# Kernel optimization log

Measured on AMD Instinct MI355X. Metric: run time of the kernel, lower is better.

Reference implementation:

```python
import jax, jax.numpy as jnp
import numpy as np

NUM_GRAPHS = 1024

def setup_inputs() -> dict:
    key = jax.random.key(0)
    k1, k2, k3, k4 = jax.random.split(key, 4)
    N, D, H = 200000, 512, 128
    h = jax.random.normal(k1, (N, D), dtype=jnp.float32)
    batch = jnp.sort(jax.random.randint(k2, (N,), 0, NUM_GRAPHS)).astype(jnp.int32)
    # gate MLP params: Linear(D,H) -> tanh -> Linear(H,1)
    W1 = jax.random.normal(k3, (D, H), dtype=jnp.float32) / np.sqrt(D)
    b1 = jnp.zeros((H,), dtype=jnp.float32)
    W2 = jax.random.normal(k4, (H, 1), dtype=jnp.float32) / np.sqrt(H)
    b2 = jnp.zeros((1,), dtype=jnp.float32)
    return {"h": h, "batch": batch, "W1": W1, "b1": b1, "W2": W2, "b2": b2}

def reference(h, batch, W1, b1, W2, b2):
    # gate MLP -> per-node logit
    logits = (jnp.tanh(h @ W1 + b1) @ W2 + b2)[:, 0]  # [N]
    # segment softmax over nodes within each graph
    seg_max = jax.ops.segment_max(logits, batch, num_segments=NUM_GRAPHS,
                                  indices_are_sorted=True)  # [G]
    ex = jnp.exp(logits - seg_max[batch])  # [N]
    denom = jax.ops.segment_sum(ex, batch, num_segments=NUM_GRAPHS,
                                indices_are_sorted=True)  # [G]
    a = ex / denom[batch]  # [N]
    # weighted scatter-add pooling
    pooled = jax.ops.segment_sum(h * a[:, None], batch, num_segments=NUM_GRAPHS,
                                 indices_are_sorted=True)  # [G, D]
    return pooled
```

## Files before the change

### kernel.cpp

```cpp
#include <hip/hip_runtime.h>
#include <hip/hip_bf16.h>

typedef __attribute__((ext_vector_type(8))) short short8;
typedef __attribute__((ext_vector_type(4))) float f32x4;

#define NGRAPHS 1024
#define D_DIM 512
#define H_DIM 128
#define BM 32
#define BMA 64

static __device__ __forceinline__ unsigned int pack_bf2(float a, float b) {
    float2 t; t.x = a; t.y = b;
    __hip_bfloat162 h = __float22bfloat162_rn(t);
    union { __hip_bfloat162 h; unsigned int u; } v;
    v.h = h;
    return v.u;
}

static __device__ __forceinline__ unsigned short f2bf(float f) {
    __hip_bfloat16 h = __float2bfloat16(f);
    union { __hip_bfloat16 h; unsigned short u; } v;
    v.h = h;
    return v.u;
}

static __device__ __forceinline__ float fast_tanh(float x) {
    float cx = fminf(fmaxf(x, -15.f), 15.f);
    float e = __expf(2.f * cx);
    return (e - 1.f) / (e + 1.f);
}

__global__ void seg_offsets_kernel(const int* __restrict__ batch, int N,
                                   int* __restrict__ off) {
    int g = blockIdx.x * 256 + threadIdx.x;
    if (g > NGRAPHS) return;
    int lo = 0, hi = N;
    while (lo < hi) {
        int mid = (lo + hi) >> 1;
        if (batch[mid] < g) lo = mid + 1;
        else hi = mid;
    }
    off[g] = lo;
}

__global__ void prep_w1t_kernel(const float* __restrict__ W1,
                                unsigned short* __restrict__ W1TF) {
    int idx = blockIdx.x * 256 + threadIdx.x;
    int e = idx & 7;
    int lane = (idx >> 3) & 63;
    int ki = (idx >> 9) & 15;
    int cgrp = idx >> 13;
    int col = cgrp * 16 + (lane & 15);
    int k = ki * 32 + (lane >> 4) * 8 + e;
    W1TF[idx] = f2bf(W1[k * H_DIM + col]);
}

__global__ __launch_bounds__(256, 4) void gate_pool_partial_kernel(
    const float* __restrict__ h, const unsigned short* __restrict__ W1TF,
    const float* __restrict__ b1, const float* __restrict__ W2,
    const int* __restrict__ batch, float* __restrict__ P,
    float* __restrict__ out, int N) {
    __shared__ unsigned short hA[BM * D_DIM];
    __shared__ float plds[4][BM];
    __shared__ float wl[BM];
    __shared__ int gb[BM];

    const int tid = threadIdx.x;
    const int lane = tid & 63;
    const int w = tid >> 6;
    const int cg = lane & 15;
    const int qg = lane >> 4;
    const int row0 = blockIdx.x * BM;

    if (tid < BM) {
        int gr = row0 + tid;
        gb[tid] = batch[gr < N ? gr : N - 1];
    }

#pragma unroll
    for (int bb = 0; bb < 2; ++bb) {
        float4 f[8];
#pragma unroll
        for (int i = 0; i < 8; ++i) {
            const int task = (bb * 8 + i) * 4 + w;
            const int row = task >> 1, half = task & 1;
            int gr = row0 + row;
            gr = gr < N ? gr : N - 1;
            f[i] = *(const float4*)(h + (size_t)gr * D_DIM + half * 256 + lane * 4);
        }
        __builtin_amdgcn_sched_barrier(0);
#pragma unroll
        for (int i = 0; i < 8; ++i) {
            const int task = (bb * 8 + i) * 4 + w;
            const int row = task >> 1, half = task & 1;
            const int unit = half * 32 + (lane >> 1);
            uint2 v;
            v.x = pack_bf2(f[i].x, f[i].y);
            v.y = pack_bf2(f[i].z, f[i].w);
            *(uint2*)&hA[row * D_DIM + ((unit ^ (row & 7)) * 8) + (lane & 1) * 4] = v;
        }
    }
    __syncthreads();

    f32x4 acc[2][2];
#pragma unroll
    for (int rf = 0; rf < 2; ++rf)
#pragma unroll
        for (int cf = 0; cf < 2; ++cf) acc[rf][cf] = (f32x4){0.f, 0.f, 0.f, 0.f};
#pragma unroll
    for (int ki = 0; ki < 16; ++ki) {
        short8 bfg[2];
#pragma unroll
        for (int cf = 0; cf < 2; ++cf)
            bfg[cf] = *(const short8*)(W1TF +
                (((w * 2 + cf) * 16 + ki) << 9) + lane * 8);
#pragma unroll
        for (int rf = 0; rf < 2; ++rf) {
            const short8 af = *(const short8*)&hA[(rf * 16 + cg) * D_DIM +
                (((4 * ki + qg) ^ (cg & 7)) * 8)];
#pragma unroll
            for (int cf = 0; cf < 2; ++cf)
                acc[rf][cf] = __builtin_amdgcn_mfma_f32_16x16x32_bf16(
                    bfg[cf], af, acc[rf][cf], 0, 0, 0);
        }
    }

    float4 b1v[2], w2v[2];
#pragma unroll
    for (int cf = 0; cf < 2; ++cf) {
        b1v[cf] = *(const float4*)&b1[(w * 2 + cf) * 16 + qg * 4];
        w2v[cf] = *(const float4*)&W2[(w * 2 + cf) * 16 + qg * 4];
    }
#pragma unroll
    for (int rf = 0; rf < 2; ++rf) {
        float p = 0.f;
#pragma unroll
        for (int cf = 0; cf < 2; ++cf) {
            p += fast_tanh(acc[rf][cf][0] + b1v[cf].x) * w2v[cf].x;
            p += fast_tanh(acc[rf][cf][1] + b1v[cf].y) * w2v[cf].y;
            p += fast_tanh(acc[rf][cf][2] + b1v[cf].z) * w2v[cf].z;
            p += fast_tanh(acc[rf][cf][3] + b1v[cf].w) * w2v[cf].w;
        }
        p += __shfl_xor(p, 16, 64);
        p += __shfl_xor(p, 32, 64);
        if (qg == 0) plds[w][rf * 16 + cg] = p;
    }
    __syncthreads();

    if (tid < BM) {
        const float l = plds[0][tid] + plds[1][tid] + plds[2][tid] + plds[3][tid];
        wl[tid] = (row0 + tid < N) ? __expf(fminf(l, 60.f)) : 0.f;
    }
    __syncthreads();

    {
        const int d0 = (tid >> 2) * 8 + (tid & 3) * 2;
        float ax = 0.f, ay = 0.f, d = 0.f;
        int curg = gb[0];
#pragma unroll 8
        for (int j = 0; j < BM; ++j) {
            const int gj = gb[j];
            if (gj != curg) {
                if (curg == gb[0]) {
                    float* rec = P + (size_t)blockIdx.x * 2 * 513;
                    rec[d0] = ax; rec[d0 + 1] = ay;
                    if (tid == 0) rec[512] = d;
                } else {
                    out[(size_t)curg * D_DIM + d0] = ax / d;
                    out[(size_t)curg * D_DIM + d0 + 1] = ay / d;
                }
                ax = 0.f; ay = 0.f; d = 0.f; curg = gj;
            }
            const float wj = wl[j];
            const unsigned int pair = *(const unsigned int*)&hA[j * D_DIM +
                (((tid >> 2) ^ (j & 7)) * 8) + (tid & 3) * 2];
            ax += wj * __uint_as_float(pair << 16);
            ay += wj * __uint_as_float(pair & 0xffff0000u);
            d += wj;
        }
        const int slot = (curg == gb[0]) ? 0 : 1;
        float* rec = P + ((size_t)blockIdx.x * 2 + slot) * 513;
        rec[d0] = ax; rec[d0 + 1] = ay;
        if (tid == 0) rec[512] = d;
        if (gb[0] == gb[BM - 1]) {
            float* r1 = P + ((size_t)blockIdx.x * 2 + 1) * 513;
            r1[d0] = 0.f; r1[d0 + 1] = 0.f;
            if (tid == 0) r1[512] = 0.f;
        }
    }
}

__global__ __launch_bounds__(512) void reduce_kernel(
    const float* __restrict__ P, const int* __restrict__ off,
    const int* __restrict__ batch, float* __restrict__ out, int N) {
    const int g = blockIdx.x;
    const int tid = threadIdx.x;
    const int s = off[g], e = off[g + 1];
    if (e <= s) { out[(size_t)g * D_DIM + tid] = 0.f; return; }
    const int t0 = s >> 5, t1 = (e - 1) >> 5;
    float sum = 0.f, den = 0.f;
    bool found = false;
    for (int b = t0; b <= t1; ++b) {
        const int fg = batch[b << 5];
        const int le = (b << 5) + 31;
        const int lg = batch[le < N ? le : N - 1];
        if (fg == g) {
            const float* rec = P + (size_t)b * 2 * 513;
            sum += rec[tid]; den += rec[512]; found = true;
        } else if (lg == g) {
            const float* rec = P + ((size_t)b * 2 + 1) * 513;
            sum += rec[tid]; den += rec[512]; found = true;
        }
    }
    if (found) out[(size_t)g * D_DIM + tid] = sum / den;
}

__global__ void zero_kernel(float* __restrict__ out, float* __restrict__ den) {
    int i = blockIdx.x * 256 + threadIdx.x;
    if (i < NGRAPHS * D_DIM) out[i] = 0.f;
    if (i < NGRAPHS) den[i] = 0.f;
}

__global__ __launch_bounds__(256) void gate_pool_atomic_kernel(
    const float* __restrict__ h, const unsigned short* __restrict__ W1TF,
    const float* __restrict__ b1, const float* __restrict__ W2,
    const int* __restrict__ batch, float* __restrict__ outnum,
    float* __restrict__ den, int N) {
    __shared__ unsigned short hA[BMA * D_DIM];
    __shared__ float plds[4][BMA];
    __shared__ float wl[BMA];
    __shared__ int gb[BMA];

    const int tid = threadIdx.x;
    const int lane = tid & 63;
    const int w = tid >> 6;
    const int cg = lane & 15;
    const int qg = lane >> 4;
    const int row0 = blockIdx.x * BMA;

    if (tid < BMA) {
        int gr = row0 + tid;
        gb[tid] = batch[gr < N ? gr : N - 1];
    }
#pragma unroll
    for (int b = 0; b < 4; ++b) {
        float4 fa[4], fb[4];
#pragma unroll
        for (int i = 0; i < 4; ++i) {
            const int fi = (b * 4 + i) * 256 + tid;
            const int r = fi >> 6, u = fi & 63;
            int gr = row0 + r;
            gr = gr < N ? gr : N - 1;
            const float* p = h + (size_t)gr * D_DIM + u * 8;
            fa[i] = *(const float4*)p;
            fb[i] = *(const float4*)(p + 4);
        }
#pragma unroll
        for (int i = 0; i < 4; ++i) {
            const int fi = (b * 4 + i) * 256 + tid;
            const int r = fi >> 6, u = fi & 63;
            uint4 val;
            val.x = pack_bf2(fa[i].x, fa[i].y);
            val.y = pack_bf2(fa[i].z, fa[i].w);
            val.z = pack_bf2(fb[i].x, fb[i].y);
            val.w = pack_bf2(fb[i].z, fb[i].w);
            *(uint4*)&hA[r * D_DIM + ((u ^ (r & 7)) * 8)] = val;
        }
    }
    __syncthreads();

    f32x4 acc[4][2];
#pragma unroll
    for (int rf = 0; rf < 4; ++rf)
#pragma unroll
        for (int cf = 0; cf < 2; ++cf) acc[rf][cf] = (f32x4){0.f, 0.f, 0.f, 0.f};
#pragma unroll
    for (int ki = 0; ki < 16; ++ki) {
        short8 bfg[2];
#pragma unroll
        for (int cf = 0; cf < 2; ++cf)
            bfg[cf] = *(const short8*)(W1TF + (((w * 2 + cf) * 16 + ki) << 9) + lane * 8);
#pragma unroll
        for (int rf = 0; rf < 4; ++rf) {
            const int row = rf * 16 + cg;
            const short8 af = *(const short8*)&hA[row * D_DIM +
                (((4 * ki + qg) ^ (row & 7)) * 8)];
#pragma unroll
            for (int cf = 0; cf < 2; ++cf)
                acc[rf][cf] = __builtin_amdgcn_mfma_f32_16x16x32_bf16(
                    af, bfg[cf], acc[rf][cf], 0, 0, 0);
        }
    }
    const float b1v0 = b1[w * 32 + cg];
    const float b1v1 = b1[w * 32 + 16 + cg];
    const float w2v0 = W2[w * 32 + cg];
    const float w2v1 = W2[w * 32 + 16 + cg];
#pragma unroll
    for (int rf = 0; rf < 4; ++rf) {
#pragma unroll
        for (int reg = 0; reg < 4; ++reg) {
            float p = fast_tanh(acc[rf][0][reg] + b1v0) * w2v0 +
                      fast_tanh(acc[rf][1][reg] + b1v1) * w2v1;
#pragma unroll
            for (int o = 1; o < 16; o <<= 1) p += __shfl_xor(p, o, 64);
            if (cg == 0) plds[w][rf * 16 + qg * 4 + reg] = p;
        }
    }
    __syncthreads();
    if (tid < BMA) {
        const float l = plds[0][tid] + plds[1][tid] + plds[2][tid] + plds[3][tid];
        wl[tid] = (row0 + tid < N) ? __expf(fminf(l, 60.f)) : 0.f;
    }
    __syncthreads();

    const int d0 = (tid >> 2) * 8 + (tid & 3) * 2;
    float ax = 0.f, ay = 0.f;
    int cur = gb[0];
#pragma unroll 8
    for (int j = 0; j < BMA; ++j) {
        const int gj = gb[j];
        if (gj != cur) {
            atomicAdd(&outnum[(size_t)cur * D_DIM + d0], ax);
            atomicAdd(&outnum[(size_t)cur * D_DIM + d0 + 1], ay);
            ax = 0.f; ay = 0.f; cur = gj;
        }
        const float wj = wl[j];
        const unsigned int pair = *(const unsigned int*)&hA[j * D_DIM +
            (((tid >> 2) ^ (j & 7)) * 8) + (tid & 3) * 2];
        ax += wj * __uint_as_float(pair << 16);
        ay += wj * __uint_as_float(pair & 0xffff0000u);
    }
    atomicAdd(&outnum[(size_t)cur * D_DIM + d0], ax);
    atomicAdd(&outnum[(size_t)cur * D_DIM + d0 + 1], ay);

    if (tid == 0) {
        float a = 0.f;
        int c2 = gb[0];
        for (int j = 0; j < BMA; ++j) {
            if (gb[j] != c2) { atomicAdd(&den[c2], a); a = 0.f; c2 = gb[j]; }
            a += wl[j];
        }
        atomicAdd(&den[c2], a);
    }
}

__global__ __launch_bounds__(512) void finalize_kernel(
    float* __restrict__ out, const float* __restrict__ den) {
    const int g = blockIdx.x;
    const float dv = den[g];
    const float v = out[(size_t)g * D_DIM + threadIdx.x];
    out[(size_t)g * D_DIM + threadIdx.x] = dv > 0.f ? v / dv : 0.f;
}

extern "C" void kernel_launch(void* const* d_in, const int* in_sizes, int n_in,
                              void* d_out, int out_size, void* d_ws, size_t ws_size,
                              hipStream_t stream) {
    const float* h = (const float*)d_in[0];
    const int* batch = (const int*)d_in[1];
    const float* W1 = (const float*)d_in[2];
    const float* b1 = (const float*)d_in[3];
    const float* W2 = (const float*)d_in[4];
    float* out = (float*)d_out;
    const int N = in_sizes[1];
    const int NB = (N + BM - 1) / BM;

    char* ws = (char*)d_ws;
    int* off = (int*)ws;
    unsigned short* W1TF = (unsigned short*)(ws + 4608);
    float* P = (float*)(ws + 135680);

    const size_t need = 135680 + (size_t)NB * 2 * 513 * 4;

    seg_offsets_kernel<<<(NGRAPHS + 256) / 256 + 1, 256, 0, stream>>>(batch, N, off);
    prep_w1t_kernel<<<(D_DIM * H_DIM) / 256, 256, 0, stream>>>(W1, W1TF);

    if (ws_size >= need) {
        gate_pool_partial_kernel<<<NB, 256, 0, stream>>>(h, W1TF, b1, W2, batch,
                                                         P, out, N);
        reduce_kernel<<<NGRAPHS, 512, 0, stream>>>(P, off, batch, out, N);
    } else {
        float* den = P;
        zero_kernel<<<(NGRAPHS * D_DIM + 255) / 256, 256, 0, stream>>>(out, den);
        gate_pool_atomic_kernel<<<(N + BMA - 1) / BMA, 256, 0, stream>>>(
            h, W1TF, b1, W2, batch, out, den, N);
        finalize_kernel<<<NGRAPHS, 512, 0, stream>>>(out, den);
    }
}
```

Measured before the change: 138.4 us.

## Process two row tiles per block, prefetching second tile during first's compute

Each block now handles two consecutive 32-row tiles. It issues global loads for the second tile's h rows into registers while the first tile's MFMA gate and pooling run, then commits them to LDS. The goal is to hide HBM latency behind compute in a memory-bound kernel. In exchange, 64 extra float registers are held per thread across the MFMA phase, which may lower occupancy under the launch bounds, and the grid is halved.

```diff
diff --git a/kernel.cpp b/kernel.cpp
--- a/kernel.cpp
+++ b/kernel.cpp
@@ -56,11 +56,125 @@
     W1TF[idx] = f2bf(W1[k * H_DIM + col]);
 }
 
-__global__ __launch_bounds__(256, 4) void gate_pool_partial_kernel(
+static __device__ __forceinline__ void stage_issue8(
+    const float* __restrict__ h, int N, int row0, int bb, int w, int lane,
+    float4* f) {
+#pragma unroll
+    for (int i = 0; i < 8; ++i) {
+        const int task = (bb * 8 + i) * 4 + w;
+        const int row = task >> 1, half = task & 1;
+        int gr = row0 + row;
+        gr = gr < N ? gr : N - 1;
+        f[i] = *(const float4*)(h + (size_t)gr * D_DIM + half * 256 + lane * 4);
+    }
+}
+
+static __device__ __forceinline__ void stage_commit8(
+    unsigned short* __restrict__ hA, int bb, int w, int lane, const float4* f) {
+#pragma unroll
+    for (int i = 0; i < 8; ++i) {
+        const int task = (bb * 8 + i) * 4 + w;
+        const int row = task >> 1, half = task & 1;
+        const int unit = half * 32 + (lane >> 1);
+        uint2 v;
+        v.x = pack_bf2(f[i].x, f[i].y);
+        v.y = pack_bf2(f[i].z, f[i].w);
+        *(uint2*)&hA[row * D_DIM + ((unit ^ (row & 7)) * 8) + (lane & 1) * 4] = v;
+    }
+}
+
+static __device__ __forceinline__ void do_mfma_epi(
+    const unsigned short* __restrict__ hA, const unsigned short* __restrict__ W1TF,
+    const float* __restrict__ b1, const float* __restrict__ W2,
+    float (*plds)[BM], int w, int lane, int cg, int qg) {
+    f32x4 acc[2][2];
+#pragma unroll
+    for (int rf = 0; rf < 2; ++rf)
+#pragma unroll
+        for (int cf = 0; cf < 2; ++cf) acc[rf][cf] = (f32x4){0.f, 0.f, 0.f, 0.f};
+#pragma unroll
+    for (int ki = 0; ki < 16; ++ki) {
+        short8 bfg[2];
+#pragma unroll
+        for (int cf = 0; cf < 2; ++cf)
+            bfg[cf] = *(const short8*)(W1TF +
+                (((w * 2 + cf) * 16 + ki) << 9) + lane * 8);
+#pragma unroll
+        for (int rf = 0; rf < 2; ++rf) {
+            const short8 af = *(const short8*)&hA[(rf * 16 + cg) * D_DIM +
+                (((4 * ki + qg) ^ (cg & 7)) * 8)];
+#pragma unroll
+            for (int cf = 0; cf < 2; ++cf)
+                acc[rf][cf] = __builtin_amdgcn_mfma_f32_16x16x32_bf16(
+                    bfg[cf], af, acc[rf][cf], 0, 0, 0);
+        }
+    }
+    float4 b1v[2], w2v[2];
+#pragma unroll
+    for (int cf = 0; cf < 2; ++cf) {
+        b1v[cf] = *(const float4*)&b1[(w * 2 + cf) * 16 + qg * 4];
+        w2v[cf] = *(const float4*)&W2[(w * 2 + cf) * 16 + qg * 4];
+    }
+#pragma unroll
+    for (int rf = 0; rf < 2; ++rf) {
+        float p = 0.f;
+#pragma unroll
+        for (int cf = 0; cf < 2; ++cf) {
+            p += fast_tanh(acc[rf][cf][0] + b1v[cf].x) * w2v[cf].x;
+            p += fast_tanh(acc[rf][cf][1] + b1v[cf].y) * w2v[cf].y;
+            p += fast_tanh(acc[rf][cf][2] + b1v[cf].z) * w2v[cf].z;
+            p += fast_tanh(acc[rf][cf][3] + b1v[cf].w) * w2v[cf].w;
+        }
+        p += __shfl_xor(p, 16, 64);
+        p += __shfl_xor(p, 32, 64);
+        if (qg == 0) plds[w][rf * 16 + cg] = p;
+    }
+}
+
+static __device__ __forceinline__ void do_pool_flush(
+    const unsigned short* __restrict__ hA, const float* __restrict__ wl,
+    const int* __restrict__ gb, float* __restrict__ P, float* __restrict__ out,
+    int t, int tid) {
+    const int d0 = (tid >> 2) * 8 + (tid & 3) * 2;
+    float ax = 0.f, ay = 0.f, d = 0.f;
+    int curg = gb[0];
+#pragma unroll 8
+    for (int j = 0; j < BM; ++j) {
+        const int gj = gb[j];
+        if (gj != curg) {
+            if (curg == gb[0]) {
+                float* rec = P + (size_t)t * 2 * 513;
+                rec[d0] = ax; rec[d0 + 1] = ay;
+                if (tid == 0) rec[512] = d;
+            } else {
+                out[(size_t)curg * D_DIM + d0] = ax / d;
+                out[(size_t)curg * D_DIM + d0 + 1] = ay / d;
+            }
+            ax = 0.f; ay = 0.f; d = 0.f; curg = gj;
+        }
+        const float wj = wl[j];
+        const unsigned int pair = *(const unsigned int*)&hA[j * D_DIM +
+            (((tid >> 2) ^ (j & 7)) * 8) + (tid & 3) * 2];
+        ax += wj * __uint_as_float(pair << 16);
+        ay += wj * __uint_as_float(pair & 0xffff0000u);
+        d += wj;
+    }
+    const int slot = (curg == gb[0]) ? 0 : 1;
+    float* rec = P + ((size_t)t * 2 + slot) * 513;
+    rec[d0] = ax; rec[d0 + 1] = ay;
+    if (tid == 0) rec[512] = d;
+    if (gb[0] == gb[BM - 1]) {
+        float* r1 = P + ((size_t)t * 2 + 1) * 513;
+        r1[d0] = 0.f; r1[d0 + 1] = 0.f;
+        if (tid == 0) r1[512] = 0.f;
+    }
+}
+
+__global__ __launch_bounds__(256, 4) void gate_pool_pipe_kernel(
     const float* __restrict__ h, const unsigned short* __restrict__ W1TF,
     const float* __restrict__ b1, const float* __restrict__ W2,
     const int* __restrict__ batch, float* __restrict__ P,
-    float* __restrict__ out, int N) {
+    float* __restrict__ out, int N, int NBtot) {
     __shared__ unsigned short hA[BM * D_DIM];
     __shared__ float plds[4][BM];
     __shared__ float wl[BM];
@@ -71,124 +185,71 @@
     const int w = tid >> 6;
     const int cg = lane & 15;
     const int qg = lane >> 4;
-    const int row0 = blockIdx.x * BM;
+
+    const int tA = blockIdx.x * 2;
+    if (tA >= NBtot) return;
+    const int tB = tA + 1;
+    const bool haveB = tB < NBtot;
+    const int row0A = tA * BM;
+    const int row0B = tB * BM;
 
     if (tid < BM) {
-        int gr = row0 + tid;
+        int gr = row0A + tid;
         gb[tid] = batch[gr < N ? gr : N - 1];
     }
 
-#pragma unroll
-    for (int bb = 0; bb < 2; ++bb) {
+    {
         float4 f[8];
-#pragma unroll
-        for (int i = 0; i < 8; ++i) {
-            const int task = (bb * 8 + i) * 4 + w;
-            const int row = task >> 1, half = task & 1;
-            int gr = row0 + row;
-            gr = gr < N ? gr : N - 1;
-            f[i] = *(const float4*)(h + (size_t)gr * D_DIM + half * 256 + lane * 4);
-        }
+        stage_issue8(h, N, row0A, 0, w, lane, f);
         __builtin_amdgcn_sched_barrier(0);
-#pragma unroll
-        for (int i = 0; i < 8; ++i) {
-            const int task = (bb * 8 + i) * 4 + w;
-            const int row = task >> 1, half = task & 1;
-            const int unit = half * 32 + (lane >> 1);
-            uint2 v;
-            v.x = pack_bf2(f[i].x, f[i].y);
-            v.y = pack_bf2(f[i].z, f[i].w);
-            *(uint2*)&hA[row * D_DIM + ((unit ^ (row & 7)) * 8) + (lane & 1) * 4] = v;
-        }
-    }
-    __syncthreads();
-
-    f32x4 acc[2][2];
-#pragma unroll
-    for (int rf = 0; rf < 2; ++rf)
-#pragma unroll
-        for (int cf = 0; cf < 2; ++cf) acc[rf][cf] = (f32x4){0.f, 0.f, 0.f, 0.f};
-#pragma unroll
-    for (int ki = 0; ki < 16; ++ki) {
-        short8 bfg[2];
-#pragma unroll
-        for (int cf = 0; cf < 2; ++cf)
-            bfg[cf] = *(const short8*)(W1TF +
-                (((w * 2 + cf) * 16 + ki) << 9) + lane * 8);
-#pragma unroll
-        for (int rf = 0; rf < 2; ++rf) {
-            const short8 af = *(const short8*)&hA[(rf * 16 + cg) * D_DIM +
-                (((4 * ki + qg) ^ (cg & 7)) * 8)];
-#pragma unroll
-            for (int cf = 0; cf < 2; ++cf)
-                acc[rf][cf] = __builtin_amdgcn_mfma_f32_16x16x32_bf16(
-                    bfg[cf], af, acc[rf][cf], 0, 0, 0);
-        }
-    }
-
-    float4 b1v[2], w2v[2];
-#pragma unroll
-    for (int cf = 0; cf < 2; ++cf) {
-        b1v[cf] = *(const float4*)&b1[(w * 2 + cf) * 16 + qg * 4];
-        w2v[cf] = *(const float4*)&W2[(w * 2 + cf) * 16 + qg * 4];
-    }
-#pragma unroll
-    for (int rf = 0; rf < 2; ++rf) {
-        float p = 0.f;
-#pragma unroll
-        for (int cf = 0; cf < 2; ++cf) {
-            p += fast_tanh(acc[rf][cf][0] + b1v[cf].x) * w2v[cf].x;
-            p += fast_tanh(acc[rf][cf][1] + b1v[cf].y) * w2v[cf].y;
-            p += fast_tanh(acc[rf][cf][2] + b1v[cf].z) * w2v[cf].z;
-            p += fast_tanh(acc[rf][cf][3] + b1v[cf].w) * w2v[cf].w;
-        }
-        p += __shfl_xor(p, 16, 64);
-        p += __shfl_xor(p, 32, 64);
-        if (qg == 0) plds[w][rf * 16 + cg] = p;
-    }
+        stage_commit8(hA, 0, w, lane, f);
+    }
+    {
+        float4 f[8];
+        stage_issue8(h, N, row0A, 1, w, lane, f);
+        __builtin_amdgcn_sched_barrier(0);
+        stage_commit8(hA, 1, w, lane, f);
+    }
+    __syncthreads();
+
+    float4 pf0[8], pf1[8];
+    if (haveB) stage_issue8(h, N, row0B, 0, w, lane, pf0);
+    __builtin_amdgcn_sched_barrier(0);
+
+    do_mfma_epi(hA, W1TF, b1, W2, plds, w, lane, cg, qg);
     __syncthreads();
 
     if (tid < BM) {
         const float l = plds[0][tid] + plds[1][tid] + plds[2][tid] + plds[3][tid];
-        wl[tid] = (row0 + tid < N) ? __expf(fminf(l, 60.f)) : 0.f;
-    }
-    __syncthreads();
-
-    {
-        const int d0 = (tid >> 2) * 8 + (tid & 3) * 2;
-        float ax = 0.f, ay = 0.f, d = 0.f;
-        int curg = gb[0];
-#pragma unroll 8
-        for (int j = 0; j < BM; ++j) {
-            const int gj = gb[j];
-            if (gj != curg) {
-                if (curg == gb[0]) {
-                    float* rec = P + (size_t)blockIdx.x * 2 * 513;
-                    rec[d0] = ax; rec[d0 + 1] = ay;
-                    if (tid == 0) rec[512] = d;
-                } else {
-                    out[(size_t)curg * D_DIM + d0] = ax / d;
-                    out[(size_t)curg * D_DIM + d0 + 1] = ay / d;
-                }
-                ax = 0.f; ay = 0.f; d = 0.f; curg = gj;
-            }
-            const float wj = wl[j];
-            const unsigned int pair = *(const unsigned int*)&hA[j * D_DIM +
-                (((tid >> 2) ^ (j & 7)) * 8) + (tid & 3) * 2];
-            ax += wj * __uint_as_float(pair << 16);
-            ay += wj * __uint_as_float(pair & 0xffff0000u);
-            d += wj;
-        }
-        const int slot = (curg == gb[0]) ? 0 : 1;
-        float* rec = P + ((size_t)blockIdx.x * 2 + slot) * 513;
-        rec[d0] = ax; rec[d0 + 1] = ay;
-        if (tid == 0) rec[512] = d;
-        if (gb[0] == gb[BM - 1]) {
-            float* r1 = P + ((size_t)blockIdx.x * 2 + 1) * 513;
-            r1[d0] = 0.f; r1[d0 + 1] = 0.f;
-            if (tid == 0) r1[512] = 0.f;
-        }
-    }
+        wl[tid] = (row0A + tid < N) ? __expf(fminf(l, 60.f)) : 0.f;
+    }
+    __syncthreads();
+
+    if (haveB) stage_issue8(h, N, row0B, 1, w, lane, pf1);
+    __builtin_amdgcn_sched_barrier(0);
+
+    do_pool_flush(hA, wl, gb, P, out, tA, tid);
+    if (!haveB) return;
+    __syncthreads();
+
+    stage_commit8(hA, 0, w, lane, pf0);
+    stage_commit8(hA, 1, w, lane, pf1);
+    if (tid < BM) {
+        int gr = row0B + tid;
+        gb[tid] = batch[gr < N ? gr : N - 1];
+    }
+    __syncthreads();
+
+    do_mfma_epi(hA, W1TF, b1, W2, plds, w, lane, cg, qg);
+    __syncthreads();
+
+    if (tid < BM) {
+        const float l = plds[0][tid] + plds[1][tid] + plds[2][tid] + plds[3][tid];
+        wl[tid] = (row0B + tid < N) ? __expf(fminf(l, 60.f)) : 0.f;
+    }
+    __syncthreads();
+
+    do_pool_flush(hA, wl, gb, P, out, tB, tid);
 }
 
 __global__ __launch_bounds__(512) void reduce_kernel(
@@ -376,8 +437,8 @@
     prep_w1t_kernel<<<(D_DIM * H_DIM) / 256, 256, 0, stream>>>(W1, W1TF);
 
     if (ws_size >= need) {
-        gate_pool_partial_kernel<<<NB, 256, 0, stream>>>(h, W1TF, b1, W2, batch,
-                                                         P, out, N);
+        gate_pool_pipe_kernel<<<(NB + 1) / 2, 256, 0, stream>>>(
+            h, W1TF, b1, W2, batch, P, out, N, NB);
         reduce_kernel<<<NGRAPHS, 512, 0, stream>>>(P, off, batch, out, N);
     } else {
         float* den = P;
```

Measured after the change: 224.7 us. 1.62x slower.

## Process 16-row tiles per single-wave block to remove block barriers

Applied to the files above, without the earlier changes.

Replaces the 4-wave, 32-row gate/pool block with a single-wave 64-thread block handling 16 rows. Graph ids and softmax weights are passed via lane shuffles instead of shared memory, and all __syncthreads are removed. Each lane now computes all 8 hidden column groups and pools 8 contiguous features. In exchange, W1 fragment loads per row double, the partial-record buffer and reduce work double, and per-CU wave occupancy may be limited by LDS per single-wave block.

```diff
diff --git a/kernel.cpp b/kernel.cpp
--- a/kernel.cpp
+++ b/kernel.cpp
@@ -7,7 +7,7 @@
 #define NGRAPHS 1024
 #define D_DIM 512
 #define H_DIM 128
-#define BM 32
+#define BW 16
 #define BMA 64
 
 static __device__ __forceinline__ unsigned int pack_bf2(float a, float b) {
@@ -56,138 +56,130 @@
     W1TF[idx] = f2bf(W1[k * H_DIM + col]);
 }
 
-__global__ __launch_bounds__(256, 4) void gate_pool_partial_kernel(
+__global__ __launch_bounds__(64, 2) void gate_pool_wave_kernel(
     const float* __restrict__ h, const unsigned short* __restrict__ W1TF,
     const float* __restrict__ b1, const float* __restrict__ W2,
     const int* __restrict__ batch, float* __restrict__ P,
     float* __restrict__ out, int N) {
-    __shared__ unsigned short hA[BM * D_DIM];
-    __shared__ float plds[4][BM];
-    __shared__ float wl[BM];
-    __shared__ int gb[BM];
-
-    const int tid = threadIdx.x;
-    const int lane = tid & 63;
-    const int w = tid >> 6;
+    __shared__ unsigned short hA[BW * D_DIM];
+
+    const int lane = threadIdx.x;
     const int cg = lane & 15;
     const int qg = lane >> 4;
-    const int row0 = blockIdx.x * BM;
-
-    if (tid < BM) {
-        int gr = row0 + tid;
-        gb[tid] = batch[gr < N ? gr : N - 1];
-    }
-
-#pragma unroll
-    for (int bb = 0; bb < 2; ++bb) {
+    const int t = blockIdx.x;
+    const int row0 = t * BW;
+
+    int gr_meta = row0 + cg;
+    const int gval = batch[gr_meta < N ? gr_meta : N - 1];
+
+#pragma unroll
+    for (int bb = 0; bb < 4; ++bb) {
         float4 f[8];
 #pragma unroll
         for (int i = 0; i < 8; ++i) {
-            const int task = (bb * 8 + i) * 4 + w;
-            const int row = task >> 1, half = task & 1;
+            const int unit = bb * 512 + i * 64 + lane;
+            const int row = unit >> 7;
+            const int uir = unit & 127;
             int gr = row0 + row;
             gr = gr < N ? gr : N - 1;
-            f[i] = *(const float4*)(h + (size_t)gr * D_DIM + half * 256 + lane * 4);
+            f[i] = *(const float4*)(h + (size_t)gr * D_DIM + uir * 4);
         }
         __builtin_amdgcn_sched_barrier(0);
 #pragma unroll
         for (int i = 0; i < 8; ++i) {
-            const int task = (bb * 8 + i) * 4 + w;
-            const int row = task >> 1, half = task & 1;
-            const int unit = half * 32 + (lane >> 1);
+            const int unit = bb * 512 + i * 64 + lane;
+            const int row = unit >> 7;
+            const int uir = unit & 127;
+            const int u16 = uir >> 1;
+            const int halfs = uir & 1;
             uint2 v;
             v.x = pack_bf2(f[i].x, f[i].y);
             v.y = pack_bf2(f[i].z, f[i].w);
-            *(uint2*)&hA[row * D_DIM + ((unit ^ (row & 7)) * 8) + (lane & 1) * 4] = v;
-        }
-    }
-    __syncthreads();
-
-    f32x4 acc[2][2];
-#pragma unroll
-    for (int rf = 0; rf < 2; ++rf)
-#pragma unroll
-        for (int cf = 0; cf < 2; ++cf) acc[rf][cf] = (f32x4){0.f, 0.f, 0.f, 0.f};
+            *(uint2*)&hA[row * D_DIM + ((u16 ^ (row & 7)) * 8) + halfs * 4] = v;
+        }
+    }
+
+    f32x4 acc[8];
+#pragma unroll
+    for (int c = 0; c < 8; ++c) acc[c] = (f32x4){0.f, 0.f, 0.f, 0.f};
 #pragma unroll
     for (int ki = 0; ki < 16; ++ki) {
-        short8 bfg[2];
-#pragma unroll
-        for (int cf = 0; cf < 2; ++cf)
-            bfg[cf] = *(const short8*)(W1TF +
-                (((w * 2 + cf) * 16 + ki) << 9) + lane * 8);
-#pragma unroll
-        for (int rf = 0; rf < 2; ++rf) {
-            const short8 af = *(const short8*)&hA[(rf * 16 + cg) * D_DIM +
-                (((4 * ki + qg) ^ (cg & 7)) * 8)];
-#pragma unroll
-            for (int cf = 0; cf < 2; ++cf)
-                acc[rf][cf] = __builtin_amdgcn_mfma_f32_16x16x32_bf16(
-                    bfg[cf], af, acc[rf][cf], 0, 0, 0);
-        }
-    }
-
-    float4 b1v[2], w2v[2];
-#pragma unroll
-    for (int cf = 0; cf < 2; ++cf) {
-        b1v[cf] = *(const float4*)&b1[(w * 2 + cf) * 16 + qg * 4];
-        w2v[cf] = *(const float4*)&W2[(w * 2 + cf) * 16 + qg * 4];
-    }
-#pragma unroll
-    for (int rf = 0; rf < 2; ++rf) {
-        float p = 0.f;
-#pragma unroll
-        for (int cf = 0; cf < 2; ++cf) {
-            p += fast_tanh(acc[rf][cf][0] + b1v[cf].x) * w2v[cf].x;
-            p += fast_tanh(acc[rf][cf][1] + b1v[cf].y) * w2v[cf].y;
-            p += fast_tanh(acc[rf][cf][2] + b1v[cf].z) * w2v[cf].z;
-            p += fast_tanh(acc[rf][cf][3] + b1v[cf].w) * w2v[cf].w;
-        }
-        p += __shfl_xor(p, 16, 64);
-        p += __shfl_xor(p, 32, 64);
-        if (qg == 0) plds[w][rf * 16 + cg] = p;
-    }
-    __syncthreads();
-
-    if (tid < BM) {
-        const float l = plds[0][tid] + plds[1][tid] + plds[2][tid] + plds[3][tid];
-        wl[tid] = (row0 + tid < N) ? __expf(fminf(l, 60.f)) : 0.f;
-    }
-    __syncthreads();
-
+        const short8 af = *(const short8*)&hA[cg * D_DIM +
+            (((4 * ki + qg) ^ (cg & 7)) * 8)];
+#pragma unroll
+        for (int c = 0; c < 8; ++c) {
+            const short8 bfg = *(const short8*)(W1TF +
+                (((c * 16 + ki) << 9)) + lane * 8);
+            acc[c] = __builtin_amdgcn_mfma_f32_16x16x32_bf16(bfg, af, acc[c],
+                                                             0, 0, 0);
+        }
+    }
+
+    float p = 0.f;
+#pragma unroll
+    for (int c = 0; c < 8; ++c) {
+        const float4 b1v = *(const float4*)&b1[c * 16 + qg * 4];
+        const float4 w2v = *(const float4*)&W2[c * 16 + qg * 4];
+        p += fast_tanh(acc[c][0] + b1v.x) * w2v.x;
+        p += fast_tanh(acc[c][1] + b1v.y) * w2v.y;
+        p += fast_tanh(acc[c][2] + b1v.z) * w2v.z;
+        p += fast_tanh(acc[c][3] + b1v.w) * w2v.w;
+    }
+    p += __shfl_xor(p, 16, 64);
+    p += __shfl_xor(p, 32, 64);
+    const float ev = (row0 + cg < N) ? __expf(fminf(p, 60.f)) : 0.f;
+
+    float ax[8];
+#pragma unroll
+    for (int e = 0; e < 8; ++e) ax[e] = 0.f;
+    float d = 0.f;
+    int curg = __shfl(gval, 0, 16);
+    const int gb0 = curg;
+    const int gb15 = __shfl(gval, 15, 16);
+
+#pragma unroll
+    for (int j = 0; j < BW; ++j) {
+        const int gj = __shfl(gval, j, 16);
+        const float wj = __shfl(ev, j, 16);
+        if (gj != curg) {
+            if (curg == gb0) {
+                float* rec = P + (size_t)t * 2 * 513;
+#pragma unroll
+                for (int e = 0; e < 8; ++e) rec[lane * 8 + e] = ax[e];
+                if (lane == 0) rec[512] = d;
+            } else {
+                float* o = out + (size_t)curg * D_DIM + lane * 8;
+                const float inv = 1.0f / d;
+#pragma unroll
+                for (int e = 0; e < 8; ++e) o[e] = ax[e] * inv;
+            }
+#pragma unroll
+            for (int e = 0; e < 8; ++e) ax[e] = 0.f;
+            d = 0.f;
+            curg = gj;
+        }
+        const short8 hv = *(const short8*)&hA[j * D_DIM +
+            ((lane ^ (j & 7)) * 8)];
+#pragma unroll
+        for (int e = 0; e < 8; ++e) {
+            const float hx = __uint_as_float(
+                ((unsigned int)(unsigned short)hv[e]) << 16);
+            ax[e] += wj * hx;
+        }
+        d += wj;
+    }
     {
-        const int d0 = (tid >> 2) * 8 + (tid & 3) * 2;
-        float ax = 0.f, ay = 0.f, d = 0.f;
-        int curg = gb[0];
-#pragma unroll 8
-        for (int j = 0; j < BM; ++j) {
-            const int gj = gb[j];
-            if (gj != curg) {
-                if (curg == gb[0]) {
-                    float* rec = P + (size_t)blockIdx.x * 2 * 513;
-                    rec[d0] = ax; rec[d0 + 1] = ay;
-                    if (tid == 0) rec[512] = d;
-                } else {
-                    out[(size_t)curg * D_DIM + d0] = ax / d;
-                    out[(size_t)curg * D_DIM + d0 + 1] = ay / d;
-                }
-                ax = 0.f; ay = 0.f; d = 0.f; curg = gj;
-            }
-            const float wj = wl[j];
-            const unsigned int pair = *(const unsigned int*)&hA[j * D_DIM +
-                (((tid >> 2) ^ (j & 7)) * 8) + (tid & 3) * 2];
-            ax += wj * __uint_as_float(pair << 16);
-            ay += wj * __uint_as_float(pair & 0xffff0000u);
-            d += wj;
-        }
-        const int slot = (curg == gb[0]) ? 0 : 1;
-        float* rec = P + ((size_t)blockIdx.x * 2 + slot) * 513;
-        rec[d0] = ax; rec[d0 + 1] = ay;
-        if (tid == 0) rec[512] = d;
-        if (gb[0] == gb[BM - 1]) {
-            float* r1 = P + ((size_t)blockIdx.x * 2 + 1) * 513;
-            r1[d0] = 0.f; r1[d0 + 1] = 0.f;
-            if (tid == 0) r1[512] = 0.f;
-        }
+        const int slot = (curg == gb0) ? 0 : 1;
+        float* rec = P + ((size_t)t * 2 + slot) * 513;
+#pragma unroll
+        for (int e = 0; e < 8; ++e) rec[lane * 8 + e] = ax[e];
+        if (lane == 0) rec[512] = d;
+    }
+    if (gb0 == gb15) {
+        float* r1 = P + ((size_t)t * 2 + 1) * 513;
+#pragma unroll
+        for (int e = 0; e < 8; ++e) r1[lane * 8 + e] = 0.f;
+        if (lane == 0) r1[512] = 0.f;
     }
 }
 
@@ -198,12 +190,12 @@
     const int tid = threadIdx.x;
     const int s = off[g], e = off[g + 1];
     if (e <= s) { out[(size_t)g * D_DIM + tid] = 0.f; return; }
-    const int t0 = s >> 5, t1 = (e - 1) >> 5;
+    const int t0 = s >> 4, t1 = (e - 1) >> 4;
     float sum = 0.f, den = 0.f;
     bool found = false;
     for (int b = t0; b <= t1; ++b) {
-        const int fg = batch[b << 5];
-        const int le = (b << 5) + 31;
+        const int fg = batch[b << 4];
+        const int le = (b << 4) + 15;
         const int lg = batch[le < N ? le : N - 1];
         if (fg == g) {
             const float* rec = P + (size_t)b * 2 * 513;
@@ -363,7 +355,7 @@
     const float* W2 = (const float*)d_in[4];
     float* out = (float*)d_out;
     const int N = in_sizes[1];
-    const int NB = (N + BM - 1) / BM;
+    const int NB = (N + BW - 1) / BW;
 
     char* ws = (char*)d_ws;
     int* off = (int*)ws;
@@ -376,8 +368,8 @@
     prep_w1t_kernel<<<(D_DIM * H_DIM) / 256, 256, 0, stream>>>(W1, W1TF);
 
     if (ws_size >= need) {
-        gate_pool_partial_kernel<<<NB, 256, 0, stream>>>(h, W1TF, b1, W2, batch,
-                                                         P, out, N);
+        gate_pool_wave_kernel<<<NB, 64, 0, stream>>>(h, W1TF, b1, W2, batch,
+                                                     P, out, N);
         reduce_kernel<<<NGRAPHS, 512, 0, stream>>>(P, off, batch, out, N);
     } else {
         float* den = P;
```

Measured after the change: 167.6 us. +21.2%, slower.
